# Kernel optimization log

Measured on AMD Instinct MI355X. Metric: run time of the kernel, lower is better.

Reference implementation:

```python
import jax, jax.numpy as jnp
import numpy as np

N = 100000
E = 1600000
IN_DIM, HID_DIM, LAT_DIM = 256, 64, 32
EPS = 1e-5


def setup_inputs() -> dict:
    key = jax.random.key(0)
    ks = jax.random.split(key, 12)
    x = jax.random.normal(ks[0], (N, IN_DIM), dtype=jnp.float32)
    edge_index = jax.random.randint(ks[1], (2, E), 0, N, dtype=jnp.int64)
    edge_weight = jax.random.uniform(ks[2], (E,), dtype=jnp.float32)
    def glorot(k, shape):
        lim = np.sqrt(6.0 / (shape[0] + shape[1]))
        return jax.random.uniform(k, shape, jnp.float32, -lim, lim)
    return {
        "x": x,
        "edge_index": edge_index,
        "edge_weight": edge_weight,
        "W1": glorot(ks[3], (IN_DIM, HID_DIM)),
        "b1": jnp.zeros((HID_DIM,), jnp.float32),
        "g1": jnp.ones((HID_DIM,), jnp.float32),
        "be1": jnp.zeros((HID_DIM,), jnp.float32),
        "W2": glorot(ks[4], (HID_DIM, LAT_DIM)),
        "b2": jnp.zeros((LAT_DIM,), jnp.float32),
        "g2": jnp.ones((LAT_DIM,), jnp.float32),
        "be2": jnp.zeros((LAT_DIM,), jnp.float32),
        "prelu_a": jnp.full((1,), 0.25, jnp.float32),  # nn.PReLU default init
        "Wr": glorot(ks[5], (IN_DIM, LAT_DIM)),
        "br": jnp.zeros((LAT_DIM,), jnp.float32),
    }


def _gcn_norm(edge_index, edge_weight):
    # PyG gcn_norm: add self-loops (w=1), symmetric D^-1/2 A_hat D^-1/2
    row, col = edge_index[0], edge_index[1]
    loop = jnp.arange(N, dtype=edge_index.dtype)
    row = jnp.concatenate([row, loop])
    col = jnp.concatenate([col, loop])
    w = jnp.concatenate([edge_weight, jnp.ones((N,), edge_weight.dtype)])
    deg = jax.ops.segment_sum(w, col, num_segments=N)
    dinv = jnp.where(deg > 0, jax.lax.rsqrt(deg), 0.0)
    norm = dinv[row] * w * dinv[col]
    return row, col, norm


def _gcn_conv(x, row, col, norm, W, b):
    h = x @ W  # transform before aggregation (PyG GCNConv)
    msg = h[row] * norm[:, None]  # [E+N, F] gather + scale
    out = jax.ops.segment_sum(msg, col, num_segments=N)  # scatter-add
    return out + b


def _batchnorm(x, gamma, beta):
    mean = jnp.mean(x, axis=0)
    var = jnp.mean((x - mean) ** 2, axis=0)  # biased, training-mode
    return gamma * (x - mean) * jax.lax.rsqrt(var + EPS) + beta


def reference(x, edge_index, edge_weight, W1, b1, g1, be1, W2, b2, g2, be2, prelu_a, Wr, br):
    row, col, norm = _gcn_norm(edge_index, edge_weight)
    x_initial = x @ Wr + br  # residual transform
    h = _gcn_conv(x, row, col, norm, W1, b1)
    h = _batchnorm(h, g1, be1)
    h = jnp.where(h >= 0, h, prelu_a[0] * h)  # PReLU (single slope)
    # dropout: identity (eval mode)
    h = _gcn_conv(h, row, col, norm, W2, b2)
    h = _batchnorm(h, g2, be2)
    return h + x_initial
```

## Files before the change

kernel.cpp:

```cpp
#include <hip/hip_runtime.h>
#include <hip/hip_bf16.h>

#define IN_DIM 256
#define HID 64
#define LAT 32
#define EPS 1e-5f
#define THREADS 256

typedef __attribute__((ext_vector_type(8))) short bf16x8;
typedef __attribute__((ext_vector_type(4))) float f32x4;

static inline int cdiv(int a, int b){ return (a + b - 1) / b; }

static __device__ inline unsigned short f2bf(float f){
  __hip_bfloat16 h = __float2bfloat16(f);
  union { __hip_bfloat16 h; unsigned short u; } cv; cv.h = h; return cv.u;
}

__global__ void k_init(float* __restrict__ deg, int* __restrict__ cnt,
                       float* __restrict__ stats, int n){
  int i = blockIdx.x * blockDim.x + threadIdx.x;
  if (i < n){ deg[i] = 1.0f; cnt[i] = 0; }
  if (i < 192) stats[i] = 0.0f;
}

__global__ void k_prep(const float* __restrict__ W1, const float* __restrict__ Wr,
                       const float* __restrict__ W2, unsigned short* __restrict__ Wtg,
                       unsigned short* __restrict__ W2tg){
  int i = blockIdx.x * blockDim.x + threadIdx.x;
  if (i < 24576){
    int c = i % 96, k = i / 96;
    float v = (c < 64) ? W1[k * 64 + c] : Wr[k * 32 + (c - 64)];
    Wtg[c * 256 + k] = f2bf(v);
  } else if (i < 24576 + 2048){
    int j = i - 24576; int c = j % 32, k = j / 32;
    W2tg[c * 64 + k] = f2bf(W2[k * 32 + c]);
  }
}

__global__ void k_count(const int* __restrict__ ei, const float* __restrict__ ew,
                        float* __restrict__ deg, int* __restrict__ cnt, int E){
  int e = blockIdx.x * blockDim.x + threadIdx.x;
  if (e >= E) return;
  int c = ei[E + e];
  atomicAdd(&deg[c], ew[e]);
  atomicAdd(&cnt[c], 1);
}

__global__ void k_scan1(const int* __restrict__ cnt, int* __restrict__ offs,
                        int* __restrict__ bsum, int n){
  __shared__ int lds[256];
  int t = threadIdx.x, b = blockIdx.x;
  int base = b * 2048 + t * 8;
  int v[8]; int s = 0;
  #pragma unroll
  for (int k = 0; k < 8; k++){ int idx = base + k; v[k] = (idx < n) ? cnt[idx] : 0; s += v[k]; }
  lds[t] = s; __syncthreads();
  for (int d = 1; d < 256; d <<= 1){
    int xv = (t >= d) ? lds[t - d] : 0;
    __syncthreads();
    lds[t] += xv;
    __syncthreads();
  }
  int excl = lds[t] - s;
  #pragma unroll
  for (int k = 0; k < 8; k++){ int idx = base + k; if (idx < n) offs[idx] = excl; excl += v[k]; }
  if (t == 0) bsum[b] = lds[255];
}

__global__ void k_scan2(int* __restrict__ bsum, int nb){
  __shared__ int lds[64];
  int t = threadIdx.x;
  int s = (t < nb) ? bsum[t] : 0;
  lds[t] = s; __syncthreads();
  for (int d = 1; d < 64; d <<= 1){
    int xv = (t >= d) ? lds[t - d] : 0;
    __syncthreads();
    lds[t] += xv;
    __syncthreads();
  }
  if (t < nb) bsum[t] = lds[t] - s;
}

__global__ void k_scan3(int* __restrict__ offs, int* __restrict__ cur,
                        const int* __restrict__ bsum, float* __restrict__ deg, int n){
  int i = blockIdx.x * blockDim.x + threadIdx.x;
  if (i >= n) return;
  int o = offs[i] + bsum[i >> 11];
  offs[i] = o; cur[i] = o;
  deg[i] = rsqrtf(deg[i]);
}

__global__ void k_fill(const int* __restrict__ ei, const float* __restrict__ ew,
                       const float* __restrict__ dinv, int* __restrict__ cur,
                       int2* __restrict__ edges, int E){
  int e = blockIdx.x * blockDim.x + threadIdx.x;
  if (e >= E) return;
  int r = ei[e], c = ei[E + e];
  int pos = atomicAdd(&cur[c], 1);
  edges[pos] = make_int2(r, __float_as_int(dinv[r] * ew[e] * dinv[c]));
}

__global__ __launch_bounds__(512, 2) void k_gemm1(
    const float* __restrict__ x, const unsigned short* __restrict__ Wtg,
    const float* __restrict__ br, float* __restrict__ h1,
    float* __restrict__ xin, int n){
  __shared__ alignas(16) unsigned short Wt[96 * 264];
  int t = threadIdx.x;
  {
    const unsigned int* src = (const unsigned int*)Wtg;
    unsigned int* dst = (unsigned int*)Wt;
    for (int d = t; d < 12288; d += 512){
      int c = d >> 7, kd = d & 127;
      dst[c * 132 + kd] = src[d];
    }
  }
  __syncthreads();

  int l = t & 63, w = t >> 6;
  int lm = l & 15, lg = l >> 4;
  int row0 = blockIdx.x * 128;
  int m = row0 + w * 16 + lm;

  union U { bf16x8 v; __hip_bfloat162 h[4]; };
  bf16x8 af[8];
  {
    bool ok = m < n;
    const float4* xr = (const float4*)(x + (size_t)m * IN_DIM);
    #pragma unroll
    for (int s = 0; s < 8; s++){
      float4 a0, a1;
      if (ok){ a0 = xr[s * 8 + lg * 2]; a1 = xr[s * 8 + lg * 2 + 1]; }
      else { a0 = make_float4(0.f,0.f,0.f,0.f); a1 = a0; }
      U u;
      u.h[0] = __float22bfloat162_rn(make_float2(a0.x, a0.y));
      u.h[1] = __float22bfloat162_rn(make_float2(a0.z, a0.w));
      u.h[2] = __float22bfloat162_rn(make_float2(a1.x, a1.y));
      u.h[3] = __float22bfloat162_rn(make_float2(a1.z, a1.w));
      af[s] = u.v;
    }
  }

  f32x4 acc[6];
  #pragma unroll
  for (int i = 0; i < 6; i++) acc[i] = (f32x4){0.f, 0.f, 0.f, 0.f};

  const char* wb = (const char*)Wt + lm * 528 + lg * 16;
  #pragma unroll
  for (int s = 0; s < 8; s++){
    #pragma unroll
    for (int tt = 0; tt < 6; tt++){
      bf16x8 bf = *(const bf16x8*)(wb + tt * 8448 + s * 64);
      acc[tt] = __builtin_amdgcn_mfma_f32_16x16x32_bf16(af[s], bf, acc[tt], 0, 0, 0);
    }
  }

  float br0 = br[lm], br1 = br[16 + lm];
  #pragma unroll
  for (int tt = 0; tt < 6; tt++){
    #pragma unroll
    for (int r = 0; r < 4; r++){
      int row = row0 + w * 16 + lg * 4 + r;
      if (row >= n) continue;
      if (tt < 4) h1[(size_t)row * HID + tt * 16 + lm] = acc[tt][r];
      else xin[(size_t)row * LAT + (tt - 4) * 16 + lm] = acc[tt][r] + (tt == 4 ? br0 : br1);
    }
  }
}

template<int F>
__global__ void k_agg(const float* __restrict__ h, const int* __restrict__ offs,
                      const int* __restrict__ cnt, const int2* __restrict__ edges,
                      const float* __restrict__ dinv, float* __restrict__ out, int n){
  int gt = blockIdx.x * blockDim.x + threadIdx.x;
  int node = gt / F;
  int lane = gt & (F - 1);
  if (node >= n) return;
  float di = dinv[node];
  float acc = h[(size_t)node * F + lane] * (di * di);
  int j = offs[node];
  int e = j + cnt[node];
  for (; j + 3 < e; j += 4){
    int2 e0 = edges[j], e1 = edges[j+1], e2 = edges[j+2], e3 = edges[j+3];
    acc = fmaf(h[(size_t)e0.x * F + lane], __int_as_float(e0.y), acc);
    acc = fmaf(h[(size_t)e1.x * F + lane], __int_as_float(e1.y), acc);
    acc = fmaf(h[(size_t)e2.x * F + lane], __int_as_float(e2.y), acc);
    acc = fmaf(h[(size_t)e3.x * F + lane], __int_as_float(e3.y), acc);
  }
  for (; j < e; j++){
    int2 ee = edges[j];
    acc = fmaf(h[(size_t)ee.x * F + lane], __int_as_float(ee.y), acc);
  }
  out[(size_t)node * F + lane] = acc;
}

template<int F>
__global__ void k_bnstats(const float* __restrict__ a, float* __restrict__ sums,
                          float* __restrict__ sqs, int n){
  __shared__ float ls[256], lq[256];
  int t = threadIdx.x;
  int f = t & (F - 1);
  const int rpb = 256 / F;
  int r = blockIdx.x * rpb + t / F;
  int stride = gridDim.x * rpb;
  float s = 0.f, q = 0.f;
  for (; r < n; r += stride){
    float v = a[(size_t)r * F + f];
    s += v; q += v * v;
  }
  ls[t] = s; lq[t] = q; __syncthreads();
  if (t < F){
    for (int j = t + F; j < 256; j += F){ s += ls[j]; q += lq[j]; }
    atomicAdd(&sums[f], s);
    atomicAdd(&sqs[f], q);
  }
}

__global__ void k_bnfin(const float* __restrict__ sums, const float* __restrict__ sqs,
                        const float* __restrict__ g, const float* __restrict__ be,
                        float* __restrict__ scale, float* __restrict__ shift,
                        int n, int F){
  int f = threadIdx.x;
  if (f >= F) return;
  float inv_n = 1.0f / (float)n;
  float mean = sums[f] * inv_n;
  float var = sqs[f] * inv_n - mean * mean;
  float sc = g[f] * rsqrtf(var + EPS);
  scale[f] = sc;
  shift[f] = be[f] - mean * sc;
}

__global__ __launch_bounds__(512, 2) void k_gemm2(
    const float* __restrict__ agg1, const float* __restrict__ scale,
    const float* __restrict__ shift, const float* __restrict__ prelu_a,
    const unsigned short* __restrict__ W2tg, float* __restrict__ h2, int n){
  __shared__ alignas(16) unsigned short W2t[32 * 72];
  __shared__ float Scl[64], Shl[64];
  int t = threadIdx.x;
  {
    const unsigned int* src = (const unsigned int*)W2tg;
    unsigned int* dst = (unsigned int*)W2t;
    for (int d = t; d < 1024; d += 512){
      int c = d >> 5, kd = d & 31;
      dst[c * 36 + kd] = src[d];
    }
    if (t < 64){ Scl[t] = scale[t]; Shl[t] = shift[t]; }
  }
  __syncthreads();

  int l = t & 63, w = t >> 6;
  int lm = l & 15, lg = l >> 4;
  int row0 = blockIdx.x * 128;
  int m = row0 + w * 16 + lm;
  float al = prelu_a[0];

  union U { bf16x8 v; __hip_bfloat162 h[4]; };
  bf16x8 af[2];
  {
    bool ok = m < n;
    const float4* ar = (const float4*)(agg1 + (size_t)m * HID);
    #pragma unroll
    for (int s = 0; s < 2; s++){
      int kb = s * 32 + lg * 8;
      float4 a0, a1;
      if (ok){ a0 = ar[kb >> 2]; a1 = ar[(kb >> 2) + 1]; }
      else { a0 = make_float4(0.f,0.f,0.f,0.f); a1 = a0; }
      float4 sc0 = *(const float4*)&Scl[kb];
      float4 sc1 = *(const float4*)&Scl[kb + 4];
      float4 sh0 = *(const float4*)&Shl[kb];
      float4 sh1 = *(const float4*)&Shl[kb + 4];
      float y0 = a0.x * sc0.x + sh0.x; y0 = (y0 >= 0.f) ? y0 : al * y0;
      float y1 = a0.y * sc0.y + sh0.y; y1 = (y1 >= 0.f) ? y1 : al * y1;
      float y2 = a0.z * sc0.z + sh0.z; y2 = (y2 >= 0.f) ? y2 : al * y2;
      float y3 = a0.w * sc0.w + sh0.w; y3 = (y3 >= 0.f) ? y3 : al * y3;
      float y4 = a1.x * sc1.x + sh1.x; y4 = (y4 >= 0.f) ? y4 : al * y4;
      float y5 = a1.y * sc1.y + sh1.y; y5 = (y5 >= 0.f) ? y5 : al * y5;
      float y6 = a1.z * sc1.z + sh1.z; y6 = (y6 >= 0.f) ? y6 : al * y6;
      float y7 = a1.w * sc1.w + sh1.w; y7 = (y7 >= 0.f) ? y7 : al * y7;
      U u;
      u.h[0] = __float22bfloat162_rn(make_float2(y0, y1));
      u.h[1] = __float22bfloat162_rn(make_float2(y2, y3));
      u.h[2] = __float22bfloat162_rn(make_float2(y4, y5));
      u.h[3] = __float22bfloat162_rn(make_float2(y6, y7));
      af[s] = u.v;
    }
  }

  f32x4 acc[2];
  #pragma unroll
  for (int i = 0; i < 2; i++) acc[i] = (f32x4){0.f, 0.f, 0.f, 0.f};

  const char* wb = (const char*)W2t + lm * 144 + lg * 16;
  #pragma unroll
  for (int s = 0; s < 2; s++){
    #pragma unroll
    for (int tt = 0; tt < 2; tt++){
      bf16x8 bf = *(const bf16x8*)(wb + tt * 2304 + s * 64);
      acc[tt] = __builtin_amdgcn_mfma_f32_16x16x32_bf16(af[s], bf, acc[tt], 0, 0, 0);
    }
  }

  #pragma unroll
  for (int tt = 0; tt < 2; tt++){
    #pragma unroll
    for (int r = 0; r < 4; r++){
      int row = row0 + w * 16 + lg * 4 + r;
      if (row >= n) continue;
      h2[(size_t)row * LAT + tt * 16 + lm] = acc[tt][r];
    }
  }
}

__global__ void k_final(const float* __restrict__ agg2, const float* __restrict__ scale,
                        const float* __restrict__ shift, const float* __restrict__ xin,
                        float* __restrict__ out, int n){
  int i = blockIdx.x * blockDim.x + threadIdx.x;
  int total = n * (LAT / 4);
  if (i >= total) return;
  float4 a = ((const float4*)agg2)[i];
  float4 xi = ((const float4*)xin)[i];
  int f = (i * 4) & (LAT - 1);
  float4 o;
  o.x = a.x * scale[f+0] + shift[f+0] + xi.x;
  o.y = a.y * scale[f+1] + shift[f+1] + xi.y;
  o.z = a.z * scale[f+2] + shift[f+2] + xi.z;
  o.w = a.w * scale[f+3] + shift[f+3] + xi.w;
  ((float4*)out)[i] = o;
}

extern "C" void kernel_launch(void* const* d_in, const int* in_sizes, int n_in,
                              void* d_out, int out_size, void* d_ws, size_t ws_size,
                              hipStream_t stream){
  const float* x   = (const float*)d_in[0];
  const int*   ei  = (const int*)d_in[1];
  const float* ew  = (const float*)d_in[2];
  const float* W1  = (const float*)d_in[3];
  const float* g1  = (const float*)d_in[5];
  const float* be1 = (const float*)d_in[6];
  const float* W2  = (const float*)d_in[7];
  const float* g2  = (const float*)d_in[9];
  const float* be2 = (const float*)d_in[10];
  const float* pa  = (const float*)d_in[11];
  const float* Wr  = (const float*)d_in[12];
  const float* br  = (const float*)d_in[13];
  float* out = (float*)d_out;

  const int N = in_sizes[0] / IN_DIM;
  const int E = in_sizes[2];

  char* ws = (char*)d_ws;
  size_t o = 0;
  auto alloc = [&](size_t bytes)->char*{
    char* p = ws + o;
    o = (o + bytes + 255) & ~(size_t)255;
    return p;
  };
  float* deg   = (float*)alloc((size_t)N * 4);
  int*   cnt   = (int*)  alloc((size_t)N * 4);
  int*   offs  = (int*)  alloc((size_t)N * 4);
  int*   cur   = (int*)  alloc((size_t)N * 4);
  int*   bsum  = (int*)  alloc(64 * 4);
  float* stats = (float*)alloc(192 * 4);
  float* coef  = (float*)alloc(192 * 4);
  unsigned short* Wtg  = (unsigned short*)alloc(96 * 256 * 2);
  unsigned short* W2tg = (unsigned short*)alloc(32 * 64 * 2);
  int2*  edges = (int2*) alloc((size_t)E * 8);
  float* bufA  = (float*)alloc((size_t)N * HID * 4);
  float* bufB  = (float*)alloc((size_t)N * HID * 4);
  float* xin   = (float*)alloc((size_t)N * LAT * 4);

  float* sums1 = stats, *sqs1 = stats + 64, *sums2 = stats + 128, *sqs2 = stats + 160;
  float* sc1 = coef, *sh1 = coef + 64, *sc2 = coef + 128, *sh2 = coef + 160;

  const int NB = cdiv(N, 2048);

  k_init<<<cdiv(N, THREADS), THREADS, 0, stream>>>(deg, cnt, stats, N);
  k_prep<<<cdiv(24576 + 2048, THREADS), THREADS, 0, stream>>>(W1, Wr, W2, Wtg, W2tg);
  k_count<<<cdiv(E, THREADS), THREADS, 0, stream>>>(ei, ew, deg, cnt, E);
  k_scan1<<<NB, 256, 0, stream>>>(cnt, offs, bsum, N);
  k_scan2<<<1, 64, 0, stream>>>(bsum, NB);
  k_scan3<<<cdiv(N, THREADS), THREADS, 0, stream>>>(offs, cur, bsum, deg, N);
  k_fill<<<cdiv(E, THREADS), THREADS, 0, stream>>>(ei, ew, deg, cur, edges, E);

  k_gemm1<<<cdiv(N, 128), 512, 0, stream>>>(x, Wtg, br, bufA, xin, N);
  k_agg<HID><<<cdiv(N * HID, THREADS), THREADS, 0, stream>>>(bufA, offs, cnt, edges, deg, bufB, N);
  k_bnstats<HID><<<256, 256, 0, stream>>>(bufB, sums1, sqs1, N);
  k_bnfin<<<1, 64, 0, stream>>>(sums1, sqs1, g1, be1, sc1, sh1, N, HID);
  k_gemm2<<<cdiv(N, 128), 512, 0, stream>>>(bufB, sc1, sh1, pa, W2tg, bufA, N);
  k_agg<LAT><<<cdiv(N * LAT, THREADS), THREADS, 0, stream>>>(bufA, offs, cnt, edges, deg, bufB, N);
  k_bnstats<LAT><<<256, 256, 0, stream>>>(bufB, sums2, sqs2, N);
  k_bnfin<<<1, 32, 0, stream>>>(sums2, sqs2, g2, be2, sc2, sh2, N, LAT);
  k_final<<<cdiv(N * LAT / 4, THREADS), THREADS, 0, stream>>>(bufB, sc2, sh2, xin, out, N);
}
```

Baseline: 617.6 us.

## Store gathered features in bf16 and pack degree/count into one 64-bit atomic

The pre-aggregation feature buffers written by both GEMMs are stored as bf16 instead of fp32, halving the bytes moved by the random neighbour gathers in the aggregation kernels. The degree sum and edge count are packed into one 64-bit integer, with the weight in 20-bit fixed point, so each edge needs a single atomic instead of two. The aggregation end offset is read from the post-fill cursor, which drops the count array. Risks are precision loss from bf16 features and from fixed-point weight quantisation in the normalisation, plus possible overflow if weight sums get large.

Measured after the change: 536.2 us. 13.2% less time.

```diff
diff --git a/kernel.cpp b/kernel.cpp
--- a/kernel.cpp
+++ b/kernel.cpp
@@ -16,11 +16,14 @@
   __hip_bfloat16 h = __float2bfloat16(f);
   union { __hip_bfloat16 h; unsigned short u; } cv; cv.h = h; return cv.u;
 }
-
-__global__ void k_init(float* __restrict__ deg, int* __restrict__ cnt,
+static __device__ inline float bf2f(unsigned short u){
+  return __uint_as_float((unsigned)u << 16);
+}
+
+__global__ void k_init(unsigned long long* __restrict__ degcnt,
                        float* __restrict__ stats, int n){
   int i = blockIdx.x * blockDim.x + threadIdx.x;
-  if (i < n){ deg[i] = 1.0f; cnt[i] = 0; }
+  if (i < n) degcnt[i] = 0ULL;
   if (i < 192) stats[i] = 0.0f;
 }
 
@@ -39,22 +42,27 @@
 }
 
 __global__ void k_count(const int* __restrict__ ei, const float* __restrict__ ew,
-                        float* __restrict__ deg, int* __restrict__ cnt, int E){
+                        unsigned long long* __restrict__ degcnt, int E){
   int e = blockIdx.x * blockDim.x + threadIdx.x;
   if (e >= E) return;
   int c = ei[E + e];
-  atomicAdd(&deg[c], ew[e]);
-  atomicAdd(&cnt[c], 1);
-}
-
-__global__ void k_scan1(const int* __restrict__ cnt, int* __restrict__ offs,
-                        int* __restrict__ bsum, int n){
+  unsigned long long pack = (1ULL << 32) |
+      (unsigned long long)__float2uint_rn(ew[e] * 1048576.0f);
+  atomicAdd(&degcnt[c], pack);
+}
+
+__global__ void k_scan1(const unsigned long long* __restrict__ degcnt,
+                        int* __restrict__ offs, int* __restrict__ bsum, int n){
   __shared__ int lds[256];
   int t = threadIdx.x, b = blockIdx.x;
   int base = b * 2048 + t * 8;
   int v[8]; int s = 0;
   #pragma unroll
-  for (int k = 0; k < 8; k++){ int idx = base + k; v[k] = (idx < n) ? cnt[idx] : 0; s += v[k]; }
+  for (int k = 0; k < 8; k++){
+    int idx = base + k;
+    v[k] = (idx < n) ? (int)(degcnt[idx] >> 32) : 0;
+    s += v[k];
+  }
   lds[t] = s; __syncthreads();
   for (int d = 1; d < 256; d <<= 1){
     int xv = (t >= d) ? lds[t - d] : 0;
@@ -83,12 +91,15 @@
 }
 
 __global__ void k_scan3(int* __restrict__ offs, int* __restrict__ cur,
-                        const int* __restrict__ bsum, float* __restrict__ deg, int n){
+                        const int* __restrict__ bsum,
+                        const unsigned long long* __restrict__ degcnt,
+                        float* __restrict__ dinv, int n){
   int i = blockIdx.x * blockDim.x + threadIdx.x;
   if (i >= n) return;
   int o = offs[i] + bsum[i >> 11];
   offs[i] = o; cur[i] = o;
-  deg[i] = rsqrtf(deg[i]);
+  float wsum = (float)(unsigned)(degcnt[i] & 0xFFFFFFFFu) * (1.0f / 1048576.0f);
+  dinv[i] = rsqrtf(1.0f + wsum);
 }
 
 __global__ void k_fill(const int* __restrict__ ei, const float* __restrict__ ew,
@@ -103,7 +114,7 @@
 
 __global__ __launch_bounds__(512, 2) void k_gemm1(
     const float* __restrict__ x, const unsigned short* __restrict__ Wtg,
-    const float* __restrict__ br, float* __restrict__ h1,
+    const float* __restrict__ br, unsigned short* __restrict__ h1,
     float* __restrict__ xin, int n){
   __shared__ alignas(16) unsigned short Wt[96 * 264];
   int t = threadIdx.x;
@@ -162,34 +173,34 @@
     for (int r = 0; r < 4; r++){
       int row = row0 + w * 16 + lg * 4 + r;
       if (row >= n) continue;
-      if (tt < 4) h1[(size_t)row * HID + tt * 16 + lm] = acc[tt][r];
+      if (tt < 4) h1[(size_t)row * HID + tt * 16 + lm] = f2bf(acc[tt][r]);
       else xin[(size_t)row * LAT + (tt - 4) * 16 + lm] = acc[tt][r] + (tt == 4 ? br0 : br1);
     }
   }
 }
 
 template<int F>
-__global__ void k_agg(const float* __restrict__ h, const int* __restrict__ offs,
-                      const int* __restrict__ cnt, const int2* __restrict__ edges,
+__global__ void k_agg(const unsigned short* __restrict__ h, const int* __restrict__ offs,
+                      const int* __restrict__ endo, const int2* __restrict__ edges,
                       const float* __restrict__ dinv, float* __restrict__ out, int n){
   int gt = blockIdx.x * blockDim.x + threadIdx.x;
   int node = gt / F;
   int lane = gt & (F - 1);
   if (node >= n) return;
   float di = dinv[node];
-  float acc = h[(size_t)node * F + lane] * (di * di);
+  float acc = bf2f(h[(size_t)node * F + lane]) * (di * di);
   int j = offs[node];
-  int e = j + cnt[node];
+  int e = endo[node];
   for (; j + 3 < e; j += 4){
     int2 e0 = edges[j], e1 = edges[j+1], e2 = edges[j+2], e3 = edges[j+3];
-    acc = fmaf(h[(size_t)e0.x * F + lane], __int_as_float(e0.y), acc);
-    acc = fmaf(h[(size_t)e1.x * F + lane], __int_as_float(e1.y), acc);
-    acc = fmaf(h[(size_t)e2.x * F + lane], __int_as_float(e2.y), acc);
-    acc = fmaf(h[(size_t)e3.x * F + lane], __int_as_float(e3.y), acc);
+    acc = fmaf(bf2f(h[(size_t)e0.x * F + lane]), __int_as_float(e0.y), acc);
+    acc = fmaf(bf2f(h[(size_t)e1.x * F + lane]), __int_as_float(e1.y), acc);
+    acc = fmaf(bf2f(h[(size_t)e2.x * F + lane]), __int_as_float(e2.y), acc);
+    acc = fmaf(bf2f(h[(size_t)e3.x * F + lane]), __int_as_float(e3.y), acc);
   }
   for (; j < e; j++){
     int2 ee = edges[j];
-    acc = fmaf(h[(size_t)ee.x * F + lane], __int_as_float(ee.y), acc);
+    acc = fmaf(bf2f(h[(size_t)ee.x * F + lane]), __int_as_float(ee.y), acc);
   }
   out[(size_t)node * F + lane] = acc;
 }
@@ -233,7 +244,7 @@
 __global__ __launch_bounds__(512, 2) void k_gemm2(
     const float* __restrict__ agg1, const float* __restrict__ scale,
     const float* __restrict__ shift, const float* __restrict__ prelu_a,
-    const unsigned short* __restrict__ W2tg, float* __restrict__ h2, int n){
+    const unsigned short* __restrict__ W2tg, unsigned short* __restrict__ h2, int n){
   __shared__ alignas(16) unsigned short W2t[32 * 72];
   __shared__ float Scl[64], Shl[64];
   int t = threadIdx.x;
@@ -306,7 +317,7 @@
     for (int r = 0; r < 4; r++){
       int row = row0 + w * 16 + lg * 4 + r;
       if (row >= n) continue;
-      h2[(size_t)row * LAT + tt * 16 + lm] = acc[tt][r];
+      h2[(size_t)row * LAT + tt * 16 + lm] = f2bf(acc[tt][r]);
     }
   }
 }
@@ -355,8 +366,8 @@
     o = (o + bytes + 255) & ~(size_t)255;
     return p;
   };
-  float* deg   = (float*)alloc((size_t)N * 4);
-  int*   cnt   = (int*)  alloc((size_t)N * 4);
+  unsigned long long* degcnt = (unsigned long long*)alloc((size_t)N * 8);
+  float* dinv  = (float*)alloc((size_t)N * 4);
   int*   offs  = (int*)  alloc((size_t)N * 4);
   int*   cur   = (int*)  alloc((size_t)N * 4);
   int*   bsum  = (int*)  alloc(64 * 4);
@@ -365,7 +376,7 @@
   unsigned short* Wtg  = (unsigned short*)alloc(96 * 256 * 2);
   unsigned short* W2tg = (unsigned short*)alloc(32 * 64 * 2);
   int2*  edges = (int2*) alloc((size_t)E * 8);
-  float* bufA  = (float*)alloc((size_t)N * HID * 4);
+  unsigned short* bufA = (unsigned short*)alloc((size_t)N * HID * 2);
   float* bufB  = (float*)alloc((size_t)N * HID * 4);
   float* xin   = (float*)alloc((size_t)N * LAT * 4);
 
@@ -374,20 +385,20 @@
 
   const int NB = cdiv(N, 2048);
 
-  k_init<<<cdiv(N, THREADS), THREADS, 0, stream>>>(deg, cnt, stats, N);
+  k_init<<<cdiv(N, THREADS), THREADS, 0, stream>>>(degcnt, stats, N);
   k_prep<<<cdiv(24576 + 2048, THREADS), THREADS, 0, stream>>>(W1, Wr, W2, Wtg, W2tg);
-  k_count<<<cdiv(E, THREADS), THREADS, 0, stream>>>(ei, ew, deg, cnt, E);
-  k_scan1<<<NB, 256, 0, stream>>>(cnt, offs, bsum, N);
+  k_count<<<cdiv(E, THREADS), THREADS, 0, stream>>>(ei, ew, degcnt, E);
+  k_scan1<<<NB, 256, 0, stream>>>(degcnt, offs, bsum, N);
   k_scan2<<<1, 64, 0, stream>>>(bsum, NB);
-  k_scan3<<<cdiv(N, THREADS), THREADS, 0, stream>>>(offs, cur, bsum, deg, N);
-  k_fill<<<cdiv(E, THREADS), THREADS, 0, stream>>>(ei, ew, deg, cur, edges, E);
+  k_scan3<<<cdiv(N, THREADS), THREADS, 0, stream>>>(offs, cur, bsum, degcnt, dinv, N);
+  k_fill<<<cdiv(E, THREADS), THREADS, 0, stream>>>(ei, ew, dinv, cur, edges, E);
 
   k_gemm1<<<cdiv(N, 128), 512, 0, stream>>>(x, Wtg, br, bufA, xin, N);
-  k_agg<HID><<<cdiv(N * HID, THREADS), THREADS, 0, stream>>>(bufA, offs, cnt, edges, deg, bufB, N);
+  k_agg<HID><<<cdiv(N * HID, THREADS), THREADS, 0, stream>>>(bufA, offs, cur, edges, dinv, bufB, N);
   k_bnstats<HID><<<256, 256, 0, stream>>>(bufB, sums1, sqs1, N);
   k_bnfin<<<1, 64, 0, stream>>>(sums1, sqs1, g1, be1, sc1, sh1, N, HID);
   k_gemm2<<<cdiv(N, 128), 512, 0, stream>>>(bufB, sc1, sh1, pa, W2tg, bufA, N);
-  k_agg<LAT><<<cdiv(N * LAT, THREADS), THREADS, 0, stream>>>(bufA, offs, cnt, edges, deg, bufB, N);
+  k_agg<LAT><<<cdiv(N * LAT, THREADS), THREADS, 0, stream>>>(bufA, offs, cur, edges, dinv, bufB, N);
   k_bnstats<LAT><<<256, 256, 0, stream>>>(bufB, sums2, sqs2, N);
   k_bnfin<<<1, 32, 0, stream>>>(sums2, sqs2, g2, be2, sc2, sh2, N, LAT);
   k_final<<<cdiv(N * LAT / 4, THREADS), THREADS, 0, stream>>>(bufB, sc2, sh2, xin, out, N);
```
